# Kernel tuning notes

Measured on AMD Instinct MI355X. Metric: run time of the kernel, lower is better.

Reference implementation:

```python
import jax, jax.numpy as jnp
import numpy as np

N_NODES = 100000


def _lightgcn_layer(x, src, dst, norm):
    # message: norm * x[src]; aggregate: mean over incoming edges at dst
    msg = norm[:, None] * x[src]                                   # [E+N, D]
    s = jax.ops.segment_sum(msg, dst, num_segments=N_NODES)        # [N, D]
    cnt = jax.ops.segment_sum(jnp.ones_like(norm), dst, num_segments=N_NODES)
    return s / cnt[:, None]                                        # deg>=1 due to self-loops


def _graph_embeddings(emb, edge_index):
    n = emb.shape[0]
    loop = jnp.arange(n, dtype=edge_index.dtype)
    src = jnp.concatenate([edge_index[0], loop])                   # self-loops appended
    dst = jnp.concatenate([edge_index[1], loop])
    deg = jax.ops.segment_sum(jnp.ones(src.shape[0], emb.dtype), src, num_segments=N_NODES)
    dis = deg ** -0.5
    norm = dis[src] * dis[dst]
    x = emb
    acc = emb
    for _ in range(2):  # num_layers
        x = _lightgcn_layer(x, src, dst, norm)
        acc = acc + x
    return acc / 3.0  # mean over (num_layers + 1) embeddings


def setup_inputs() -> dict:
    key = jax.random.key(0)
    k1, k2, k3, k4 = jax.random.split(key, 4)
    emb = jax.random.normal(k1, (N_NODES, 128), dtype=jnp.float32) * 0.02
    edge_index = jax.random.randint(k2, (2, 600000), 0, N_NODES, dtype=jnp.int64)
    items = jax.random.randint(k3, (4096, 1), 0, N_NODES, dtype=jnp.int64)
    samples = jax.random.randint(k4, (4096, 100), 0, N_NODES, dtype=jnp.int64)
    return {"emb": emb, "edge_index": edge_index, "items": items, "samples": samples}


def reference(emb, edge_index, items, samples):
    embeddings = _graph_embeddings(emb, edge_index)                # [N, D]
    item_emb = embeddings[items]                                   # [B, 1, D]
    sample_emb = embeddings[samples]                               # [B, S, D]
    scores = jnp.einsum('bod,bsd->bos', item_emb, sample_emb)      # [B, 1, S]
    return scores.squeeze(1)                                       # [B, S]
```

## Files before the change

### kernel.cpp

```cpp
#include <hip/hip_runtime.h>

#define NN 100000
#define D 128
#define W 32

__device__ __forceinline__ unsigned short f2bf(float f) {
    unsigned u = __float_as_uint(f);
    u += 0x7FFF + ((u >> 16) & 1);
    return (unsigned short)(u >> 16);
}
__device__ __forceinline__ float bflo(unsigned u) { return __uint_as_float(u << 16); }
__device__ __forceinline__ float bfhi(unsigned u) { return __uint_as_float(u & 0xFFFF0000u); }
__device__ __forceinline__ unsigned pack2(float a, float b) {
    return (unsigned)f2bf(a) | ((unsigned)f2bf(b) << 16);
}
__device__ __forceinline__ void addrow(float* acc, const uint4 v, float w) {
    acc[0] += w * bflo(v.x); acc[1] += w * bfhi(v.x);
    acc[2] += w * bflo(v.y); acc[3] += w * bfhi(v.y);
    acc[4] += w * bflo(v.z); acc[5] += w * bfhi(v.z);
    acc[6] += w * bflo(v.w); acc[7] += w * bfhi(v.w);
}

__global__ __launch_bounds__(256) void hetero_kernel(const int* __restrict__ src,
                                                     const int* __restrict__ dst,
                                                     const float* __restrict__ emb,
                                                     int* __restrict__ deg,
                                                     int* __restrict__ fillc,
                                                     int* __restrict__ ell,
                                                     unsigned short* __restrict__ y0h,
                                                     int E, int EB, int total, int total8) {
    int b = blockIdx.x;
    int lo = (int)(((long long)b * EB) / total);
    int hi = (int)(((long long)(b + 1) * EB) / total);
    if (hi > lo) {
        int e = lo * 256 + threadIdx.x;
        if (e < E) {
            int s = src[e], d = dst[e];
            atomicAdd(&deg[s], 1);
            int pos = atomicAdd(&fillc[d], 1);
            if (pos < W) ell[(size_t)d * W + pos] = s;
        }
    } else {
        int t = (b - hi) * 256 + threadIdx.x;
        if (t < total8) {
            const float4 a = ((const float4*)emb)[t * 2];
            const float4 c = ((const float4*)emb)[t * 2 + 1];
            uint4 o;
            o.x = pack2(a.x, a.y);
            o.y = pack2(a.z, a.w);
            o.z = pack2(c.x, c.y);
            o.w = pack2(c.z, c.w);
            ((uint4*)y0h)[t] = o;
        }
    }
}

__global__ __launch_bounds__(256) void gather1_kernel(const int* __restrict__ ell,
                                                      const int* __restrict__ fillc,
                                                      const int* __restrict__ deg,
                                                      const unsigned short* __restrict__ y0h,
                                                      unsigned short* __restrict__ y1h, int n) {
    unsigned t = blockIdx.x * 256u + threadIdx.x;
    unsigned i = t >> 4, q = t & 15u;
    if (i >= (unsigned)n) return;
    int len = fillc[i];
    int lenc = len > W ? W : len;
    const int* base = ell + (size_t)i * W;
    float wd = rsqrtf((float)deg[i] + 1.0f);
    const uint4 ph = *(const uint4*)(y0h + (size_t)i * D + q * 8);
    float acc[8] = {0.f, 0.f, 0.f, 0.f, 0.f, 0.f, 0.f, 0.f};
    addrow(acc, ph, wd);
    int j = 0;
    for (; j + 4 <= lenc; j += 4) {
        const int4 ss = *(const int4*)(base + j);
        float w0 = rsqrtf((float)deg[ss.x] + 1.0f);
        float w1 = rsqrtf((float)deg[ss.y] + 1.0f);
        float w2 = rsqrtf((float)deg[ss.z] + 1.0f);
        float w3 = rsqrtf((float)deg[ss.w] + 1.0f);
        const uint4 v0 = *(const uint4*)(y0h + (size_t)ss.x * D + q * 8);
        const uint4 v1 = *(const uint4*)(y0h + (size_t)ss.y * D + q * 8);
        const uint4 v2 = *(const uint4*)(y0h + (size_t)ss.z * D + q * 8);
        const uint4 v3 = *(const uint4*)(y0h + (size_t)ss.w * D + q * 8);
        addrow(acc, v0, w0);
        addrow(acc, v1, w1);
        addrow(acc, v2, w2);
        addrow(acc, v3, w3);
    }
    for (; j < lenc; ++j) {
        int s0 = base[j];
        float w0 = rsqrtf((float)deg[s0] + 1.0f);
        const uint4 v0 = *(const uint4*)(y0h + (size_t)s0 * D + q * 8);
        addrow(acc, v0, w0);
    }
    float ci = 1.0f / (float)(len + 1);
    float f1 = ci * wd * wd;
    uint4 o;
    o.x = pack2(f1 * acc[0], f1 * acc[1]);
    o.y = pack2(f1 * acc[2], f1 * acc[3]);
    o.z = pack2(f1 * acc[4], f1 * acc[5]);
    o.w = pack2(f1 * acc[6], f1 * acc[7]);
    *(uint4*)(y1h + (size_t)i * D + q * 8) = o;
}

__global__ __launch_bounds__(256) void gather2_kernel(const int* __restrict__ ell,
                                                      const int* __restrict__ fillc,
                                                      const int* __restrict__ deg,
                                                      const unsigned short* __restrict__ y1h,
                                                      const float* __restrict__ emb,
                                                      unsigned short* __restrict__ finh, int n) {
    unsigned t = blockIdx.x * 256u + threadIdx.x;
    unsigned i = t >> 4, q = t & 15u;
    if (i >= (unsigned)n) return;
    int len = fillc[i];
    int lenc = len > W ? W : len;
    const int* base = ell + (size_t)i * W;
    const uint4 ph = *(const uint4*)(y1h + (size_t)i * D + q * 8);
    float self[8];
    self[0] = bflo(ph.x); self[1] = bfhi(ph.x);
    self[2] = bflo(ph.y); self[3] = bfhi(ph.y);
    self[4] = bflo(ph.z); self[5] = bfhi(ph.z);
    self[6] = bflo(ph.w); self[7] = bfhi(ph.w);
    float acc[8];
    #pragma unroll
    for (int k = 0; k < 8; ++k) acc[k] = self[k];
    int j = 0;
    for (; j + 4 <= lenc; j += 4) {
        const int4 ss = *(const int4*)(base + j);
        const uint4 v0 = *(const uint4*)(y1h + (size_t)ss.x * D + q * 8);
        const uint4 v1 = *(const uint4*)(y1h + (size_t)ss.y * D + q * 8);
        const uint4 v2 = *(const uint4*)(y1h + (size_t)ss.z * D + q * 8);
        const uint4 v3 = *(const uint4*)(y1h + (size_t)ss.w * D + q * 8);
        addrow(acc, v0, 1.0f);
        addrow(acc, v1, 1.0f);
        addrow(acc, v2, 1.0f);
        addrow(acc, v3, 1.0f);
    }
    for (; j < lenc; ++j) {
        int s0 = base[j];
        const uint4 v0 = *(const uint4*)(y1h + (size_t)s0 * D + q * 8);
        addrow(acc, v0, 1.0f);
    }
    float dp1 = (float)deg[i] + 1.0f;
    float wd = rsqrtf(dp1);
    float wdi = sqrtf(dp1);
    float ci = 1.0f / (float)(len + 1);
    float g = ci * wd;
    const float4 e0 = *(const float4*)(emb + (size_t)i * D + q * 8);
    const float4 e1 = *(const float4*)(emb + (size_t)i * D + q * 8 + 4);
    const float k3 = 1.0f / 3.0f;
    float r[8];
    r[0] = (e0.x + self[0] * wdi + g * acc[0]) * k3;
    r[1] = (e0.y + self[1] * wdi + g * acc[1]) * k3;
    r[2] = (e0.z + self[2] * wdi + g * acc[2]) * k3;
    r[3] = (e0.w + self[3] * wdi + g * acc[3]) * k3;
    r[4] = (e1.x + self[4] * wdi + g * acc[4]) * k3;
    r[5] = (e1.y + self[5] * wdi + g * acc[5]) * k3;
    r[6] = (e1.z + self[6] * wdi + g * acc[6]) * k3;
    r[7] = (e1.w + self[7] * wdi + g * acc[7]) * k3;
    uint4 o;
    o.x = pack2(r[0], r[1]);
    o.y = pack2(r[2], r[3]);
    o.z = pack2(r[4], r[5]);
    o.w = pack2(r[6], r[7]);
    *(uint4*)(finh + (size_t)i * D + q * 8) = o;
}

__global__ __launch_bounds__(256) void scores_kernel(const unsigned short* __restrict__ finh,
                                                     const int* __restrict__ items,
                                                     const int* __restrict__ samples,
                                                     float* __restrict__ out, int S) {
    __shared__ float it[D];
    int b = blockIdx.x;
    if (threadIdx.x < 64) {
        unsigned u = ((const unsigned*)(finh + (size_t)items[b] * D))[threadIdx.x];
        it[threadIdx.x * 2] = bflo(u);
        it[threadIdx.x * 2 + 1] = bfhi(u);
    }
    __syncthreads();
    int g = threadIdx.x >> 4, lane = threadIdx.x & 15;
    float w[8];
    #pragma unroll
    for (int k = 0; k < 8; ++k) w[k] = it[lane * 8 + k];
    int s = g;
    for (; s + 16 < S; s += 32) {
        int node0 = samples[b * S + s];
        int node1 = samples[b * S + s + 16];
        const uint4 v0 = *(const uint4*)(finh + (size_t)node0 * D + lane * 8);
        const uint4 v1 = *(const uint4*)(finh + (size_t)node1 * D + lane * 8);
        float a0 = w[0] * bflo(v0.x) + w[1] * bfhi(v0.x) + w[2] * bflo(v0.y) + w[3] * bfhi(v0.y)
                 + w[4] * bflo(v0.z) + w[5] * bfhi(v0.z) + w[6] * bflo(v0.w) + w[7] * bfhi(v0.w);
        float a1 = w[0] * bflo(v1.x) + w[1] * bfhi(v1.x) + w[2] * bflo(v1.y) + w[3] * bfhi(v1.y)
                 + w[4] * bflo(v1.z) + w[5] * bfhi(v1.z) + w[6] * bflo(v1.w) + w[7] * bfhi(v1.w);
        #pragma unroll
        for (int o = 8; o; o >>= 1) {
            a0 += __shfl_xor(a0, o);
            a1 += __shfl_xor(a1, o);
        }
        if (lane == 0) {
            out[b * S + s] = a0;
            out[b * S + s + 16] = a1;
        }
    }
    if (s < S) {
        int node = samples[b * S + s];
        const uint4 v = *(const uint4*)(finh + (size_t)node * D + lane * 8);
        float a = w[0] * bflo(v.x) + w[1] * bfhi(v.x) + w[2] * bflo(v.y) + w[3] * bfhi(v.y)
                + w[4] * bflo(v.z) + w[5] * bfhi(v.z) + w[6] * bflo(v.w) + w[7] * bfhi(v.w);
        #pragma unroll
        for (int o = 8; o; o >>= 1) a += __shfl_xor(a, o);
        if (lane == 0) out[b * S + s] = a;
    }
}

extern "C" void kernel_launch(void* const* d_in, const int* in_sizes, int n_in,
                              void* d_out, int out_size, void* d_ws, size_t ws_size,
                              hipStream_t stream) {
    const float* emb = (const float*)d_in[0];
    const int* ei = (const int*)d_in[1];
    const int* items = (const int*)d_in[2];
    const int* samples = (const int*)d_in[3];
    float* out = (float*)d_out;

    const int E = in_sizes[1] / 2;
    const int B = in_sizes[2];
    const int S = in_sizes[3] / B;
    const int* src = ei;
    const int* dst = ei + E;

    int* deg = (int*)d_ws;
    int* fillc = deg + NN;
    int* ell = fillc + NN;
    unsigned short* y0h = (unsigned short*)(ell + (size_t)NN * W);
    unsigned short* y1h = y0h + (size_t)NN * D;
    unsigned short* finh = y1h + (size_t)NN * D;

    hipMemsetAsync(deg, 0, 2 * NN * sizeof(int), stream);

    const int EB = (E + 255) / 256;
    const int total8 = NN * D / 8;
    const int CB = (total8 + 255) / 256;
    const int total = EB + CB;
    hetero_kernel<<<total, 256, 0, stream>>>(src, dst, emb, deg, fillc, ell, y0h,
                                             E, EB, total, total8);

    const int gblocks = (NN * 16 + 255) / 256;
    gather1_kernel<<<gblocks, 256, 0, stream>>>(ell, fillc, deg, y0h, y1h, NN);
    gather2_kernel<<<gblocks, 256, 0, stream>>>(ell, fillc, deg, y1h, emb, finh, NN);

    scores_kernel<<<B, 256, 0, stream>>>(finh, items, samples, out, S);
}
```

Baseline: 152.9 us.

## Compute source degrees with LDS-privatized range histograms instead of global atomics

Removes the per-edge global atomicAdd on deg from the hetero kernel. The degree is now built by a two-pass histogram: each block keeps an LDS counter array for a 16K-node range over one slice of the edges, and a reduction kernel sums the 14 partial arrays. This is meant to cut contention on global atomics. In exchange it adds two kernel launches, reads src seven times in total, and writes and reads back a 14xN partial buffer.

```diff
diff --git a/kernel.cpp b/kernel.cpp
--- a/kernel.cpp
+++ b/kernel.cpp
@@ -3,6 +3,9 @@
 #define NN 100000
 #define D 128
 #define W 32
+#define RS 16384
+#define NRANGE 7
+#define NSPLIT 14
 
 __device__ __forceinline__ unsigned short f2bf(float f) {
     unsigned u = __float_as_uint(f);
@@ -24,7 +27,6 @@
 __global__ __launch_bounds__(256) void hetero_kernel(const int* __restrict__ src,
                                                      const int* __restrict__ dst,
                                                      const float* __restrict__ emb,
-                                                     int* __restrict__ deg,
                                                      int* __restrict__ fillc,
                                                      int* __restrict__ ell,
                                                      unsigned short* __restrict__ y0h,
@@ -36,7 +38,6 @@
         int e = lo * 256 + threadIdx.x;
         if (e < E) {
             int s = src[e], d = dst[e];
-            atomicAdd(&deg[s], 1);
             int pos = atomicAdd(&fillc[d], 1);
             if (pos < W) ell[(size_t)d * W + pos] = s;
         }
@@ -53,6 +54,34 @@
             ((uint4*)y0h)[t] = o;
         }
     }
+}
+
+__global__ __launch_bounds__(256) void histA_kernel(const int* __restrict__ src,
+                                                    int* __restrict__ part, int E) {
+    __shared__ int h[RS];
+    int r = blockIdx.x / NSPLIT, c = blockIdx.x % NSPLIT;
+    int lo = r * RS, hi = min(lo + RS, NN);
+    for (int t = threadIdx.x; t < RS; t += 256) h[t] = 0;
+    __syncthreads();
+    int chunk = (E + NSPLIT - 1) / NSPLIT;
+    int e0 = c * chunk, e1 = min(e0 + chunk, E);
+    for (int e = e0 + (int)threadIdx.x; e < e1; e += 256) {
+        int s = src[e];
+        if (s >= lo && s < hi) atomicAdd(&h[s - lo], 1);
+    }
+    __syncthreads();
+    for (int t = threadIdx.x; t < hi - lo; t += 256)
+        part[(size_t)c * NN + lo + t] = h[t];
+}
+
+__global__ __launch_bounds__(256) void histB_kernel(const int* __restrict__ part,
+                                                    int* __restrict__ deg, int n) {
+    int i = blockIdx.x * 256 + threadIdx.x;
+    if (i >= n) return;
+    int s = 0;
+    #pragma unroll
+    for (int c = 0; c < NSPLIT; ++c) s += part[(size_t)c * NN + i];
+    deg[i] = s;
 }
 
 __global__ __launch_bounds__(256) void gather1_kernel(const int* __restrict__ ell,
@@ -230,18 +259,22 @@
     int* deg = (int*)d_ws;
     int* fillc = deg + NN;
     int* ell = fillc + NN;
-    unsigned short* y0h = (unsigned short*)(ell + (size_t)NN * W);
+    int* part = ell + (size_t)NN * W;
+    unsigned short* y0h = (unsigned short*)(part + (size_t)NSPLIT * NN);
     unsigned short* y1h = y0h + (size_t)NN * D;
     unsigned short* finh = y1h + (size_t)NN * D;
 
-    hipMemsetAsync(deg, 0, 2 * NN * sizeof(int), stream);
+    hipMemsetAsync(fillc, 0, NN * sizeof(int), stream);
 
     const int EB = (E + 255) / 256;
     const int total8 = NN * D / 8;
     const int CB = (total8 + 255) / 256;
     const int total = EB + CB;
-    hetero_kernel<<<total, 256, 0, stream>>>(src, dst, emb, deg, fillc, ell, y0h,
+    hetero_kernel<<<total, 256, 0, stream>>>(src, dst, emb, fillc, ell, y0h,
                                              E, EB, total, total8);
+
+    histA_kernel<<<NRANGE * NSPLIT, 256, 0, stream>>>(src, part, E);
+    histB_kernel<<<(NN + 255) / 256, 256, 0, stream>>>(part, deg, NN);
 
     const int gblocks = (NN * 16 + 255) / 256;
     gather1_kernel<<<gblocks, 256, 0, stream>>>(ell, fillc, deg, y0h, y1h, NN);
```

After: 185.1 us. +21.1%, slower.
